# Optimization experiments

Hardware: AMD Instinct MI355X
Metric: run time of the kernel (lower is better)

## Reference

```python
import jax, jax.numpy as jnp
import numpy as np

B, N, CACHE = 2, 2048, 512
D_MODEL, N_HEADS, HEAD_DIM, FF, KSZ = 768, 12, 64, 3072, 31
EPS = 1e-5


def rmsnorm(x, w):
    return x * jax.lax.rsqrt(jnp.mean(x * x, axis=-1, keepdims=True) + EPS) * w


def rope(x, pos):
    # x: [B, T, H, D], pos: [T] (absolute positions incl. cache offset)
    half = x.shape[-1] // 2
    inv = 1.0 / (10000.0 ** (jnp.arange(half, dtype=jnp.float32) / half))
    ang = pos.astype(jnp.float32)[:, None] * inv[None, :]           # [T, half]
    cos = jnp.concatenate([jnp.cos(ang), jnp.cos(ang)], -1)[None, :, None, :]
    sin = jnp.concatenate([jnp.sin(ang), jnp.sin(ang)], -1)[None, :, None, :]
    x1, x2 = x[..., :half], x[..., half:]
    rot = jnp.concatenate([-x2, x1], -1)
    return x * cos + rot * sin


def setup_inputs() -> dict:
    key = jax.random.key(0)
    ks = jax.random.split(key, 16)
    w = lambda k, shape: jax.random.normal(k, shape, jnp.float32) * 0.02
    kk = jax.random.split(ks[15], 16)
    return {
        "x": jax.random.normal(ks[0], (B, N, D_MODEL), jnp.float32),
        "attn_mask": jnp.ones((B, CACHE + N), bool),
        "pad_mask": jnp.zeros((B, N), bool),
        "length": N,
        "cached_kv": jax.random.normal(ks[1], (B, CACHE, 2, N_HEADS, HEAD_DIM), jnp.float32),
        "ff1_norm_w": jnp.ones((D_MODEL,), jnp.float32),
        "ff1_w1": w(ks[2], (D_MODEL, FF)), "ff1_b1": jnp.zeros((FF,), jnp.float32),
        "ff1_w2": w(ks[3], (FF, D_MODEL)), "ff1_b2": jnp.zeros((D_MODEL,), jnp.float32),
        "attn_norm_w": jnp.ones((D_MODEL,), jnp.float32),
        "qkv_w": w(ks[4], (D_MODEL, 3 * N_HEADS * HEAD_DIM)),
        "out_w": w(ks[5], (N_HEADS * HEAD_DIM, D_MODEL)),
        "q_norm_w": jnp.ones((HEAD_DIM,), jnp.float32),
        "k_norm_w": jnp.ones((HEAD_DIM,), jnp.float32),
        "conv_norm_w": jnp.ones((D_MODEL,), jnp.float32),
        "pw1_w": w(ks[6], (D_MODEL, 2 * D_MODEL)), "pw1_b": jnp.zeros((2 * D_MODEL,), jnp.float32),
        "dw_w": w(ks[7], (D_MODEL, KSZ)), "dw_b": jnp.zeros((D_MODEL,), jnp.float32),
        "bn_g": jnp.ones((D_MODEL,), jnp.float32), "bn_b": jnp.zeros((D_MODEL,), jnp.float32),
        "pw2_w": w(ks[8], (D_MODEL, D_MODEL)), "pw2_b": jnp.zeros((D_MODEL,), jnp.float32),
        "ff2_norm_w": jnp.ones((D_MODEL,), jnp.float32),
        "ff2_w1": w(kk[0], (D_MODEL, FF)), "ff2_b1": jnp.zeros((FF,), jnp.float32),
        "ff2_w2": w(kk[1], (FF, D_MODEL)), "ff2_b2": jnp.zeros((D_MODEL,), jnp.float32),
        "out_norm_w": jnp.ones((D_MODEL,), jnp.float32),
    }


def _ff(x, nw, w1, b1, w2, b2):
    h = jax.nn.gelu(rmsnorm(x, nw) @ w1 + b1)        # FusedMLP: gelu(tanh approx)
    return 0.5 * (h @ w2 + b2)                        # Scale(0.5, ...)


def _attention(x, pad_mask, attn_mask, cached_kv, nw, qkv_w, out_w, qnw, knw):
    y = rmsnorm(x, nw)
    y = jnp.where(pad_mask[..., None], 0.0, y)
    qkv = (y @ qkv_w).reshape(B, N, N_HEADS, HEAD_DIM, 3)  # (h d qkv) layout
    q, k, v = qkv[..., 0], qkv[..., 1], qkv[..., 2]
    q = rmsnorm(q, qnw)
    k = rmsnorm(k, knw)
    k_full = jnp.concatenate([cached_kv[:, :, 0], k], axis=1)  # [B, KV, H, D]
    v_full = jnp.concatenate([cached_kv[:, :, 1], v], axis=1)
    kv_to_cache = jnp.stack([k_full, v_full], axis=2)          # [B, KV, 2, H, D]
    kv_len = k_full.shape[1]
    pos = jnp.arange(kv_len)
    k_rot = rope(k_full, pos)
    q_rot = rope(q, pos[kv_len - N:])
    scale = 1.0 / jnp.sqrt(jnp.asarray(HEAD_DIM, jnp.float32))
    scores = jnp.einsum('bqhd,bkhd->bhqk', q_rot, k_rot) * scale
    scores = jnp.where(attn_mask[:, None, None, :], scores, jnp.finfo(scores.dtype).min)
    attn = jax.nn.softmax(scores, axis=-1)
    out = jnp.einsum('bhqk,bkhd->bqhd', attn, v_full).reshape(B, N, N_HEADS * HEAD_DIM)
    out = jnp.where(pad_mask[..., None], 0.0, out)
    return out @ out_w, kv_to_cache


def _conv(x, pad_mask, nw, pw1_w, pw1_b, dw_w, dw_b, bn_g, bn_b, pw2_w, pw2_b):
    y = rmsnorm(x, nw)
    y = jnp.where(pad_mask[..., None], 0.0, y)
    y = y @ pw1_w + pw1_b                             # pointwise conv1
    a, b = jnp.split(y, 2, axis=-1)
    y = a * jax.nn.sigmoid(b)                          # GLU
    rhs = dw_w.T[:, None, :]                           # [K, 1, C] (WIO, depthwise)
    y = jax.lax.conv_general_dilated(
        y, rhs, (1,), [(KSZ // 2, KSZ // 2)],
        dimension_numbers=('NWC', 'WIO', 'NWC'),
        feature_group_count=D_MODEL) + dw_b
    m = jnp.mean(y, axis=(0, 1))                       # batch(re)norm, train-mode stats
    v = jnp.var(y, axis=(0, 1))
    y = (y - m) * jax.lax.rsqrt(v + EPS) * bn_g + bn_b
    y = y * jax.nn.sigmoid(y)                          # SiLU
    return y @ pw2_w + pw2_b


def reference(x, attn_mask, pad_mask, length, cached_kv,
              ff1_norm_w, ff1_w1, ff1_b1, ff1_w2, ff1_b2,
              attn_norm_w, qkv_w, out_w, q_norm_w, k_norm_w,
              conv_norm_w, pw1_w, pw1_b, dw_w, dw_b, bn_g, bn_b, pw2_w, pw2_b,
              ff2_norm_w, ff2_w1, ff2_b1, ff2_w2, ff2_b2, out_norm_w):
    x = _ff(x, ff1_norm_w, ff1_w1, ff1_b1, ff1_w2, ff1_b2) + x
    attn_out, kv_to_cache = _attention(x, pad_mask, attn_mask, cached_kv,
                                       attn_norm_w, qkv_w, out_w, q_norm_w, k_norm_w)
    x = attn_out + x
    # NOTE: source code has no residual add around the conv block
    x = _conv(x, pad_mask, conv_norm_w, pw1_w, pw1_b, dw_w, dw_b, bn_g, bn_b, pw2_w, pw2_b)
    x = _ff(x, ff2_norm_w, ff2_w1, ff2_b1, ff2_w2, ff2_b2) + x
    x = rmsnorm(x, out_norm_w)
    return x, kv_to_cache
```

## Files before the change

### kernel.cpp

```cpp
#include <hip/hip_runtime.h>
#include <hip/hip_bf16.h>
#include <math.h>

namespace {
constexpr int Bc   = 2;
constexpr int Nn   = 2048;
constexpr int CACHE= 512;
constexpr int KVL  = 2560;
constexpr int DM   = 768;
constexpr int NH   = 12;
constexpr int HD   = 64;
constexpr int FFD  = 3072;
constexpr int RR   = Bc * Nn;
}
#define EPSF 1e-5f

typedef unsigned short u16;
typedef __bf16 bf16x8 __attribute__((ext_vector_type(8)));
typedef float  f32x4  __attribute__((ext_vector_type(4)));
typedef u16    u16x8  __attribute__((ext_vector_type(8)));
typedef u16    u16x4  __attribute__((ext_vector_type(4)));

#define GPTR(p) ((const __attribute__((address_space(1))) void*)(p))
#define LPTR(p) ((__attribute__((address_space(3))) void*)(p))

__device__ __forceinline__ float geluf(float x) {
  float x3 = x * x * x;
  float t  = tanhf(0.7978845608028654f * (x + 0.044715f * x3));
  return 0.5f * x * (1.0f + t);
}
__device__ __forceinline__ float sigmoidf_(float x) {
  return 1.0f / (1.0f + __expf(-x));
}
__device__ __forceinline__ u16 f2bf(float x) {
  union { float f; unsigned u; } v; v.f = x;
  unsigned r = (v.u + 0x7fffu + ((v.u >> 16) & 1u)) >> 16;
  return (u16)r;
}
__device__ __forceinline__ float bf2f(u16 u) {
  union { unsigned u; float f; } v; v.u = ((unsigned)u) << 16;
  return v.f;
}

template<bool BF>
__global__ __launch_bounds__(256) void k_rmsnorm2(const float* __restrict__ in,
                                                  const float* __restrict__ w,
                                                  void* __restrict__ outv, int D) {
  const int row = blockIdx.x;
  const float* x = in + (size_t)row * D;
  float ss = 0.f;
  for (int i = threadIdx.x; i < D; i += 256) { float v = x[i]; ss = fmaf(v, v, ss); }
  __shared__ float red[5];
#pragma unroll
  for (int off = 32; off > 0; off >>= 1) ss += __shfl_down(ss, off, 64);
  if ((threadIdx.x & 63) == 0) red[threadIdx.x >> 6] = ss;
  __syncthreads();
  if (threadIdx.x == 0) red[4] = red[0] + red[1] + red[2] + red[3];
  __syncthreads();
  const float scale = rsqrtf(red[4] * (1.0f / (float)D) + EPSF);
  for (int i = threadIdx.x; i < D; i += 256) {
    const float v = x[i] * scale * w[i];
    if (BF) ((u16*)outv)[(size_t)row * D + i] = f2bf(v);
    else    ((float*)outv)[(size_t)row * D + i] = v;
  }
}

__global__ __launch_bounds__(256) void k_wt(const float* __restrict__ W,
                                            u16* __restrict__ Wt, int K, int N) {
  __shared__ __align__(16) u16 T[64][72];
  const int nb = blockIdx.x * 64;
  const int kb = blockIdx.y * 64;
#pragma unroll
  for (int p = 0; p < 4; ++p) {
    const int r = p * 16 + (threadIdx.x >> 4);
    const int c = (threadIdx.x & 15) * 4;
    float4 v = *(const float4*)(W + (size_t)(kb + r) * N + nb + c);
    T[c + 0][r] = f2bf(v.x); T[c + 1][r] = f2bf(v.y);
    T[c + 2][r] = f2bf(v.z); T[c + 3][r] = f2bf(v.w);
  }
  __syncthreads();
  const int cc = (threadIdx.x & 7) * 8;
#pragma unroll
  for (int p = 0; p < 2; ++p) {
    const int rr = p * 32 + (threadIdx.x >> 3);
    *(u16x8*)(Wt + (size_t)(nb + rr) * K + kb + cc) = *(const u16x8*)&T[rr][cc];
  }
}

template<int BN, int MODE, bool OUTBF>
__global__ __launch_bounds__(256) void k_gemm_mfma(const u16* __restrict__ A,
                                                   const u16* __restrict__ Wt,
                                                   const float* __restrict__ bias,
                                                   const float* __restrict__ res,
                                                   void* __restrict__ Cv,
                                                   int K, int Nc) {
  constexpr int BM = 128, BK = 64;
  constexpr int CT = BN / 32;
  __shared__ __align__(16) u16 As[BM * BK];
  __shared__ __align__(16) u16 Bs[BN * BK];
  const int lane = threadIdx.x & 63;
  const int w    = threadIdx.x >> 6;
  const int rowBase = blockIdx.y * BM;
  const int colBase = blockIdx.x * BN;
  const int l15 = lane & 15, quad = lane >> 4;
  const int wr = w >> 1, wc = w & 1;
  const int sw = l15 & 7;

  f32x4 acc[4][CT];
#pragma unroll
  for (int i = 0; i < 4; ++i)
#pragma unroll
    for (int j = 0; j < CT; ++j) acc[i][j] = (f32x4){0.f, 0.f, 0.f, 0.f};

  for (int k0 = 0; k0 < K; k0 += BK) {
#pragma unroll
    for (int s = 0; s < 4; ++s) {
      const int cbase = (w * 4 + s) * 64;
      const int c = cbase + lane;
      const int r = c >> 3;
      const int kc = (c & 7) ^ (r & 7);
      __builtin_amdgcn_global_load_lds(
          GPTR(A + (size_t)(rowBase + r) * K + k0 + kc * 8),
          LPTR((char*)As + (size_t)cbase * 16), 16, 0, 0);
    }
#pragma unroll
    for (int s = 0; s < BN / 32; ++s) {
      const int cbase = (w * (BN / 32) + s) * 64;
      const int c = cbase + lane;
      const int r = c >> 3;
      const int kc = (c & 7) ^ (r & 7);
      __builtin_amdgcn_global_load_lds(
          GPTR(Wt + (size_t)(colBase + r) * K + k0 + kc * 8),
          LPTR((char*)Bs + (size_t)cbase * 16), 16, 0, 0);
    }
    __syncthreads();

#pragma unroll
    for (int kk = 0; kk < 2; ++kk) {
      bf16x8 aF[4], bF[CT];
#pragma unroll
      for (int rt = 0; rt < 4; ++rt) {
        const int row = wr * 64 + rt * 16 + l15;
        aF[rt] = *(const bf16x8*)&As[row * BK + (((kk * 4 + quad) ^ sw) * 8)];
      }
#pragma unroll
      for (int ct = 0; ct < CT; ++ct) {
        const int row = wc * (BN / 2) + ct * 16 + l15;
        bF[ct] = *(const bf16x8*)&Bs[row * BK + (((kk * 4 + quad) ^ sw) * 8)];
      }
#pragma unroll
      for (int rt = 0; rt < 4; ++rt)
#pragma unroll
        for (int ct = 0; ct < CT; ++ct)
          acc[rt][ct] = __builtin_amdgcn_mfma_f32_16x16x32_bf16(aF[rt], bF[ct],
                                                                acc[rt][ct], 0, 0, 0);
    }
    __syncthreads();
  }

#pragma unroll
  for (int ct = 0; ct < CT; ++ct) {
    const int col = colBase + wc * (BN / 2) + ct * 16 + l15;
    const float bv = bias ? bias[col] : 0.f;
#pragma unroll
    for (int rt = 0; rt < 4; ++rt) {
#pragma unroll
      for (int r = 0; r < 4; ++r) {
        const int row = rowBase + wr * 64 + rt * 16 + quad * 4 + r;
        float v = acc[rt][ct][r] + bv;
        if (MODE == 1) v = geluf(v);
        else if (MODE == 2) v = 0.5f * v + res[(size_t)row * Nc + col];
        else if (MODE == 3) v = v + res[(size_t)row * Nc + col];
        if (OUTBF) ((u16*)Cv)[(size_t)row * Nc + col] = f2bf(v);
        else       ((float*)Cv)[(size_t)row * Nc + col] = v;
      }
    }
  }
}

__global__ __launch_bounds__(768) void k_qkv_post(const float* __restrict__ qkv,
                                                  const float* __restrict__ qw,
                                                  const float* __restrict__ kw,
                                                  u16* __restrict__ qbf,
                                                  u16* __restrict__ krotbf,
                                                  float* __restrict__ kvout) {
  const int row = blockIdx.x;
  const int b = row >> 11;
  const int n = row & 2047;
  const int h = threadIdx.x >> 6;
  const int d = threadIdx.x & 63;
  const float* src = qkv + (size_t)row * (3 * DM) + h * 192 + d * 3;
  const float q = src[0], k = src[1], v = src[2];
  float sq = q * q, sk = k * k;
#pragma unroll
  for (int off = 32; off > 0; off >>= 1) {
    sq += __shfl_xor(sq, off, 64);
    sk += __shfl_xor(sk, off, 64);
  }
  const float qs = rsqrtf(sq * (1.0f / 64.0f) + EPSF);
  const float ks = rsqrtf(sk * (1.0f / 64.0f) + EPSF);
  const float qn = q * qs * qw[d];
  const float kn = k * ks * kw[d];
  const size_t kvbase = ((size_t)b * KVL + (CACHE + n)) * (2 * DM) + h * 64 + d;
  kvout[kvbase] = kn;
  kvout[kvbase + DM] = v;
  const int j = d & 31;
  const float inv = powf(10000.0f, -(float)j * (1.0f / 32.0f));
  float s, c;
  sincosf((float)(CACHE + n) * inv, &s, &c);
  const float oq = __shfl_xor(qn, 32, 64);
  const float ok = __shfl_xor(kn, 32, 64);
  const float rq = (d < 32) ? -oq : oq;
  const float rk = (d < 32) ? -ok : ok;
  qbf[((size_t)row * NH + h) * 64 + d] = f2bf((qn * c + rq * s) * 0.125f);
  krotbf[((size_t)(b * KVL + CACHE + n) * NH + h) * 64 + d] = f2bf(kn * c + rk * s);
}

__global__ __launch_bounds__(768) void k_cache_prep(const float* __restrict__ cached,
                                                    float* __restrict__ kvout,
                                                    u16* __restrict__ krotbf) {
  const int row = blockIdx.x;
  const int b = row / CACHE, t = row - b * CACHE;
  const int h = threadIdx.x >> 6;
  const int d = threadIdx.x & 63;
  const float k = cached[((size_t)row * 2 + 0) * DM + h * 64 + d];
  const float v = cached[((size_t)row * 2 + 1) * DM + h * 64 + d];
  const size_t kb = ((size_t)b * KVL + t) * (2 * DM) + h * 64 + d;
  kvout[kb] = k;
  kvout[kb + DM] = v;
  const int j = d & 31;
  const float inv = powf(10000.0f, -(float)j * (1.0f / 32.0f));
  float s, c;
  sincosf((float)t * inv, &s, &c);
  const float ok = __shfl_xor(k, 32, 64);
  const float rk = (d < 32) ? -ok : ok;
  krotbf[((size_t)(b * KVL + t) * NH + h) * 64 + d] = f2bf(k * c + rk * s);
}

__global__ __launch_bounds__(256) void k_vt(const float* __restrict__ kvout,
                                            u16* __restrict__ vtbf) {
  __shared__ __align__(16) u16 T[64][72];
  const int bh = blockIdx.x / 40;
  const int tb = blockIdx.x % 40;
  const int b = bh / NH, h = bh % NH;
  const int t0 = tb * 64;
  {
    const int tloc = threadIdx.x >> 2;
    const int dg = (threadIdx.x & 3) * 16;
    const float* src = kvout + ((size_t)b * KVL + t0 + tloc) * (2 * DM) + DM + h * 64 + dg;
    float4 v0 = *(const float4*)(src);
    float4 v1 = *(const float4*)(src + 4);
    float4 v2 = *(const float4*)(src + 8);
    float4 v3 = *(const float4*)(src + 12);
    T[dg + 0][tloc] = f2bf(v0.x);  T[dg + 1][tloc] = f2bf(v0.y);
    T[dg + 2][tloc] = f2bf(v0.z);  T[dg + 3][tloc] = f2bf(v0.w);
    T[dg + 4][tloc] = f2bf(v1.x);  T[dg + 5][tloc] = f2bf(v1.y);
    T[dg + 6][tloc] = f2bf(v1.z);  T[dg + 7][tloc] = f2bf(v1.w);
    T[dg + 8][tloc] = f2bf(v2.x);  T[dg + 9][tloc] = f2bf(v2.y);
    T[dg + 10][tloc] = f2bf(v2.z); T[dg + 11][tloc] = f2bf(v2.w);
    T[dg + 12][tloc] = f2bf(v3.x); T[dg + 13][tloc] = f2bf(v3.y);
    T[dg + 14][tloc] = f2bf(v3.z); T[dg + 15][tloc] = f2bf(v3.w);
  }
  __syncthreads();
  const int d = threadIdx.x >> 2;
  const int kg = (threadIdx.x & 3) * 16;
  u16x8 a = *(const u16x8*)&T[d][kg];
  u16x8 b8 = *(const u16x8*)&T[d][kg + 8];
  u16* dst = vtbf + ((size_t)(b * NH + h) * 64 + d) * KVL + t0 + kg;
  *(u16x8*)dst = a;
  *(u16x8*)(dst + 8) = b8;
}

__global__ __launch_bounds__(256) void k_attn2(const u16* __restrict__ qbf,
                                               const u16* __restrict__ krotbf,
                                               const u16* __restrict__ vtbf,
                                               float* __restrict__ Apart,
                                               float* __restrict__ lpart) {
  __shared__ __align__(16) u16 Ks[64 * 64];
  __shared__ __align__(16) u16 Vs[64 * 64];
  __shared__ __align__(16) u16 Ps[4][16][80];
  const int lane = threadIdx.x & 63;
  const int wid  = threadIdx.x >> 6;
  const int sp   = blockIdx.x & 1;
  const int rest = blockIdx.x >> 1;
  const int qblk = rest & 31;
  const int bh   = rest >> 5;
  const int b = bh / NH, h = bh % NH;
  const int q0 = qblk * 64 + wid * 16;
  const int l15 = lane & 15;
  const int quad = lane >> 4;
  const int sw = l15 & 7;

  const u16* qp = qbf + ((size_t)(b * Nn + q0 + l15) * NH + h) * 64 + quad * 8;
  const bf16x8 bQ0 = *(const bf16x8*)qp;
  const bf16x8 bQ1 = *(const bf16x8*)(qp + 32);

  f32x4 O[4] = {};
  float l_lane = 0.f;

  const u16* kbase = krotbf + ((size_t)b * KVL * NH + h) * 64;
  const u16* vbase = vtbf + ((size_t)(b * NH + h) * 64) * KVL;

  const int tbeg = sp * (KVL / 2);
  for (int t0 = tbeg; t0 < tbeg + KVL / 2; t0 += 64) {
    __syncthreads();
#pragma unroll
    for (int it = 0; it < 2; ++it) {
      const int cbase = (wid * 2 + it) * 64;
      const int c = cbase + lane;
      const int r = c >> 3;
      const int kc = (c & 7) ^ (r & 7);
      __builtin_amdgcn_global_load_lds(
          GPTR(kbase + (size_t)(t0 + r) * (NH * 64) + kc * 8),
          LPTR((char*)Ks + (size_t)cbase * 16), 16, 0, 0);
      __builtin_amdgcn_global_load_lds(
          GPTR(vbase + (size_t)r * KVL + t0 + kc * 8),
          LPTR((char*)Vs + (size_t)cbase * 16), 16, 0, 0);
    }
    __syncthreads();

#pragma unroll
    for (int nt = 0; nt < 4; ++nt) {
      const int krow = nt * 16 + l15;
      const bf16x8 aK0 = *(const bf16x8*)&Ks[krow * 64 + ((quad ^ sw) * 8)];
      const bf16x8 aK1 = *(const bf16x8*)&Ks[krow * 64 + (((4 + quad) ^ sw) * 8)];
      f32x4 cc = {};
      cc = __builtin_amdgcn_mfma_f32_16x16x32_bf16(aK0, bQ0, cc, 0, 0, 0);
      cc = __builtin_amdgcn_mfma_f32_16x16x32_bf16(aK1, bQ1, cc, 0, 0, 0);
      const float p0 = __expf(cc[0]);
      const float p1 = __expf(cc[1]);
      const float p2 = __expf(cc[2]);
      const float p3 = __expf(cc[3]);
      l_lane += (p0 + p1) + (p2 + p3);
      uint2 pk;
      pk.x = (unsigned)f2bf(p0) | ((unsigned)f2bf(p1) << 16);
      pk.y = (unsigned)f2bf(p2) | ((unsigned)f2bf(p3) << 16);
      *(uint2*)&Ps[wid][l15][nt * 16 + quad * 4] = pk;
    }
    asm volatile("s_waitcnt lgkmcnt(0)" ::: "memory");

#pragma unroll
    for (int kt = 0; kt < 2; ++kt) {
      const bf16x8 bP = *(const bf16x8*)&Ps[wid][l15][kt * 32 + quad * 8];
#pragma unroll
      for (int ot = 0; ot < 4; ++ot) {
        const int vrow = ot * 16 + l15;
        const bf16x8 aV = *(const bf16x8*)&Vs[vrow * 64 + (((kt * 4 + quad) ^ sw) * 8)];
        O[ot] = __builtin_amdgcn_mfma_f32_16x16x32_bf16(aV, bP, O[ot], 0, 0, 0);
      }
    }
  }

  l_lane += __shfl_xor(l_lane, 16, 64);
  l_lane += __shfl_xor(l_lane, 32, 64);
  const int sbh = (sp * Bc + b) * NH + h;
  if (quad == 0) lpart[(size_t)sbh * Nn + q0 + l15] = l_lane;
  float* ap = Apart + ((size_t)sbh * 64) * Nn + q0 + l15;
#pragma unroll
  for (int ot = 0; ot < 4; ++ot)
#pragma unroll
    for (int r = 0; r < 4; ++r)
      ap[(size_t)(ot * 16 + quad * 4 + r) * Nn] = O[ot][r];
}

__global__ __launch_bounds__(256) void k_attn_merge(const float* __restrict__ Apart,
                                                    const float* __restrict__ lpart,
                                                    u16* __restrict__ attnout) {
  __shared__ float T[64][65];
  __shared__ float il[64];
  const int qt = blockIdx.x & 31;
  const int bh = blockIdx.x >> 5;
  const int b = bh / NH, h = bh % NH;
  const int q0 = qt * 64;
  const int bh0 = b * NH + h;
  const int bh1 = (Bc + b) * NH + h;
  if (threadIdx.x < 64) {
    const int q = threadIdx.x;
    il[q] = 1.0f / (lpart[(size_t)bh0 * Nn + q0 + q] + lpart[(size_t)bh1 * Nn + q0 + q]);
  }
  const float* a0 = Apart + ((size_t)bh0 * 64) * Nn + q0;
  const float* a1 = Apart + ((size_t)bh1 * 64) * Nn + q0;
#pragma unroll
  for (int p = 0; p < 16; ++p) {
    const int idx = p * 256 + threadIdx.x;
    const int d = idx >> 6, q = idx & 63;
    T[q][d] = a0[(size_t)d * Nn + q] + a1[(size_t)d * Nn + q];
  }
  __syncthreads();
#pragma unroll
  for (int p = 0; p < 16; ++p) {
    const int idx = p * 256 + threadIdx.x;
    const int q = idx >> 6, d = idx & 63;
    attnout[((size_t)(b * Nn + q0 + q)) * DM + h * 64 + d] = f2bf(T[q][d] * il[q]);
  }
}

__global__ __launch_bounds__(256) void k_dwconv2(const u16* __restrict__ pw1,
                                                 const float* __restrict__ w,
                                                 const float* __restrict__ bsd,
                                                 float* __restrict__ out,
                                                 float* __restrict__ stats) {
  __shared__ float S[94][68];
  __shared__ float Wl[31][64];
  const int cb = blockIdx.x * 64;
  const int n0 = blockIdx.y * 64;
  const int b  = blockIdx.z;
  for (int idx = threadIdx.x; idx < 94 * 16; idx += 256) {
    const int r = idx >> 4, cg = (idx & 15) * 4;
    const int n = n0 - 15 + r;
    float4 v = make_float4(0.f, 0.f, 0.f, 0.f);
    if (n >= 0 && n < Nn) {
      const u16* p = pw1 + ((size_t)(b * Nn + n)) * (2 * DM) + cb + cg;
      u16x4 av = *(const u16x4*)(p);
      u16x4 gv = *(const u16x4*)(p + DM);
      v.x = bf2f(av[0]) * sigmoidf_(bf2f(gv[0]));
      v.y = bf2f(av[1]) * sigmoidf_(bf2f(gv[1]));
      v.z = bf2f(av[2]) * sigmoidf_(bf2f(gv[2]));
      v.w = bf2f(av[3]) * sigmoidf_(bf2f(gv[3]));
    }
    *(float4*)&S[r][cg] = v;
  }
  for (int idx = threadIdx.x; idx < 31 * 64; idx += 256) {
    const int c = idx & 63, tap = idx >> 6;
    Wl[tap][c] = w[(size_t)(cb + c) * 31 + tap];
  }
  __syncthreads();

  const int cg  = (threadIdx.x & 15) * 4;
  const int nl0 = threadIdx.x >> 4;
  const float4 b4 = *(const float4*)(bsd + cb + cg);
  float sum[4] = {0.f, 0.f, 0.f, 0.f};
  float sq[4]  = {0.f, 0.f, 0.f, 0.f};
#pragma unroll
  for (int p = 0; p < 4; ++p) {
    const int nl = p * 16 + nl0;
    float a0 = b4.x, a1 = b4.y, a2 = b4.z, a3 = b4.w;
#pragma unroll
    for (int t = 0; t < 31; ++t) {
      const float4 sv = *(const float4*)&S[nl + t][cg];
      const float4 wv = *(const float4*)&Wl[t][cg & 63];
      a0 = fmaf(sv.x, wv.x, a0); a1 = fmaf(sv.y, wv.y, a1);
      a2 = fmaf(sv.z, wv.z, a2); a3 = fmaf(sv.w, wv.w, a3);
    }
    *(float4*)(out + ((size_t)(b * Nn + n0 + nl)) * DM + cb + cg) =
        make_float4(a0, a1, a2, a3);
    sum[0] += a0; sum[1] += a1; sum[2] += a2; sum[3] += a3;
    sq[0] = fmaf(a0, a0, sq[0]); sq[1] = fmaf(a1, a1, sq[1]);
    sq[2] = fmaf(a2, a2, sq[2]); sq[3] = fmaf(a3, a3, sq[3]);
  }
  __syncthreads();
  *(float4*)&S[nl0][cg]      = make_float4(sum[0], sum[1], sum[2], sum[3]);
  *(float4*)&S[16 + nl0][cg] = make_float4(sq[0], sq[1], sq[2], sq[3]);
  __syncthreads();
  if (threadIdx.x < 64) {
    const int c = threadIdx.x;
    float s = 0.f, q = 0.f;
#pragma unroll
    for (int i = 0; i < 16; ++i) { s += S[i][c]; q += S[16 + i][c]; }
    atomicAdd(&stats[cb + c], s);
    atomicAdd(&stats[DM + cb + c], q);
  }
}

__global__ __launch_bounds__(256) void k_zero(float* __restrict__ p, int n) {
  const int i = blockIdx.x * 256 + threadIdx.x;
  if (i < n) p[i] = 0.f;
}

__global__ __launch_bounds__(256) void k_bn_apply(const float* __restrict__ x,
                                                  const float* __restrict__ stats,
                                                  const float* __restrict__ g,
                                                  const float* __restrict__ bb,
                                                  u16* __restrict__ out) {
  const int idx = blockIdx.x * 256 + threadIdx.x;
  const int c = idx % DM;
  const float mean = stats[c] * (1.0f / (float)RR);
  const float var = stats[DM + c] * (1.0f / (float)RR) - mean * mean;
  float y = (x[idx] - mean) * rsqrtf(var + EPSF) * g[c] + bb[c];
  out[idx] = f2bf(y * sigmoidf_(y));
}

extern "C" void kernel_launch(void* const* d_in, const int* in_sizes, int n_in,
                              void* d_out, int out_size, void* d_ws, size_t ws_size,
                              hipStream_t stream) {
  const float* x       = (const float*)d_in[0];
  const float* cached  = (const float*)d_in[4];
  const float* ff1_nw  = (const float*)d_in[5];
  const float* ff1_w1  = (const float*)d_in[6];
  const float* ff1_b1  = (const float*)d_in[7];
  const float* ff1_w2  = (const float*)d_in[8];
  const float* ff1_b2  = (const float*)d_in[9];
  const float* attn_nw = (const float*)d_in[10];
  const float* qkv_w   = (const float*)d_in[11];
  const float* out_w   = (const float*)d_in[12];
  const float* q_nw    = (const float*)d_in[13];
  const float* k_nw    = (const float*)d_in[14];
  const float* conv_nw = (const float*)d_in[15];
  const float* pw1_w   = (const float*)d_in[16];
  const float* pw1_b   = (const float*)d_in[17];
  const float* dw_w    = (const float*)d_in[18];
  const float* dw_b    = (const float*)d_in[19];
  const float* bn_g    = (const float*)d_in[20];
  const float* bn_b    = (const float*)d_in[21];
  const float* pw2_w   = (const float*)d_in[22];
  const float* pw2_b   = (const float*)d_in[23];
  const float* ff2_nw  = (const float*)d_in[24];
  const float* ff2_w1  = (const float*)d_in[25];
  const float* ff2_b1  = (const float*)d_in[26];
  const float* ff2_w2  = (const float*)d_in[27];
  const float* ff2_b2  = (const float*)d_in[28];
  const float* out_nw  = (const float*)d_in[29];

  float* out_x  = (float*)d_out;
  float* out_kv = out_x + (size_t)RR * DM;

  u16* wt_ff1w1 = (u16*)d_ws;
  u16* wt_ff1w2 = wt_ff1w1 + (size_t)3072 * 768;
  u16* wt_qkv   = wt_ff1w2 + (size_t)768 * 3072;
  u16* wt_out   = wt_qkv   + (size_t)2304 * 768;
  u16* wt_pw1   = wt_out   + (size_t)768 * 768;
  u16* wt_pw2   = wt_pw1   + (size_t)1536 * 768;
  u16* wt_ff2w1 = wt_pw2   + (size_t)768 * 768;
  u16* wt_ff2w2 = wt_ff2w1 + (size_t)3072 * 768;
  u16* abuf     = wt_ff2w2 + (size_t)768 * 3072;
  u16* hbuf     = abuf + (size_t)RR * DM;
  float* xA     = (float*)(hbuf + (size_t)RR * FFD);
  float* xB     = xA + (size_t)RR * DM;
  float* qkvbuf = xB + (size_t)RR * DM;
  u16* qbf      = (u16*)(qkvbuf + (size_t)RR * 3 * DM);
  u16* krotbf   = qbf + (size_t)RR * DM;
  u16* vtbf     = krotbf + (size_t)Bc * KVL * DM;
  float* bn_stats = (float*)(vtbf + (size_t)Bc * KVL * DM);
  float* Apart  = (float*)hbuf;
  u16* attnout  = (u16*)qkvbuf;
  float* lpart  = qkvbuf + (size_t)RR * DM;
  float* dwout  = qkvbuf;
  u16* bnout    = (u16*)(qkvbuf + (size_t)RR * DM);

  const dim3 blk(256);
  k_wt<<<dim3(48, 12), blk, 0, stream>>>(ff1_w1, wt_ff1w1, DM, FFD);
  k_wt<<<dim3(12, 48), blk, 0, stream>>>(ff1_w2, wt_ff1w2, FFD, DM);
  k_wt<<<dim3(36, 12), blk, 0, stream>>>(qkv_w, wt_qkv, DM, 3 * DM);
  k_wt<<<dim3(12, 12), blk, 0, stream>>>(out_w, wt_out, DM, DM);
  k_wt<<<dim3(24, 12), blk, 0, stream>>>(pw1_w, wt_pw1, DM, 2 * DM);
  k_wt<<<dim3(12, 12), blk, 0, stream>>>(pw2_w, wt_pw2, DM, DM);
  k_wt<<<dim3(48, 12), blk, 0, stream>>>(ff2_w1, wt_ff2w1, DM, FFD);
  k_wt<<<dim3(12, 48), blk, 0, stream>>>(ff2_w2, wt_ff2w2, FFD, DM);

  k_rmsnorm2<true><<<RR, blk, 0, stream>>>(x, ff1_nw, abuf, DM);
  k_gemm_mfma<128, 1, true><<<dim3(FFD / 128, RR / 128), blk, 0, stream>>>(
      abuf, wt_ff1w1, ff1_b1, nullptr, hbuf, DM, FFD);
  k_gemm_mfma<64, 2, false><<<dim3(DM / 64, RR / 128), blk, 0, stream>>>(
      hbuf, wt_ff1w2, ff1_b2, x, xA, FFD, DM);
  k_rmsnorm2<true><<<RR, blk, 0, stream>>>(xA, attn_nw, abuf, DM);
  k_gemm_mfma<128, 0, false><<<dim3(3 * DM / 128, RR / 128), blk, 0, stream>>>(
      abuf, wt_qkv, nullptr, nullptr, qkvbuf, DM, 3 * DM);
  k_qkv_post<<<RR, 768, 0, stream>>>(qkvbuf, q_nw, k_nw, qbf, krotbf, out_kv);
  k_cache_prep<<<Bc * CACHE, 768, 0, stream>>>(cached, out_kv, krotbf);
  k_vt<<<Bc * NH * (KVL / 64), blk, 0, stream>>>(out_kv, vtbf);
  k_attn2<<<Bc * NH * (Nn / 64) * 2, blk, 0, stream>>>(qbf, krotbf, vtbf, Apart, lpart);
  k_attn_merge<<<Bc * NH * (Nn / 64), blk, 0, stream>>>(Apart, lpart, attnout);
  k_gemm_mfma<64, 3, false><<<dim3(DM / 64, RR / 128), blk, 0, stream>>>(
      attnout, wt_out, nullptr, xA, xB, DM, DM);
  k_rmsnorm2<true><<<RR, blk, 0, stream>>>(xB, conv_nw, abuf, DM);
  k_gemm_mfma<128, 0, true><<<dim3(2 * DM / 128, RR / 128), blk, 0, stream>>>(
      abuf, wt_pw1, pw1_b, nullptr, hbuf, DM, 2 * DM);
  k_zero<<<6, blk, 0, stream>>>(bn_stats, 2 * DM);
  k_dwconv2<<<dim3(DM / 64, Nn / 64, Bc), blk, 0, stream>>>(hbuf, dw_w, dw_b,
                                                            dwout, bn_stats);
  k_bn_apply<<<RR * DM / 256, blk, 0, stream>>>(dwout, bn_stats, bn_g, bn_b, bnout);
  k_gemm_mfma<64, 0, false><<<dim3(DM / 64, RR / 128), blk, 0, stream>>>(
      bnout, wt_pw2, pw2_b, nullptr, xA, DM, DM);
  k_rmsnorm2<true><<<RR, blk, 0, stream>>>(xA, ff2_nw, abuf, DM);
  k_gemm_mfma<128, 1, true><<<dim3(FFD / 128, RR / 128), blk, 0, stream>>>(
      abuf, wt_ff2w1, ff2_b1, nullptr, hbuf, DM, FFD);
  k_gemm_mfma<64, 2, false><<<dim3(DM / 64, RR / 128), blk, 0, stream>>>(
      hbuf, wt_ff2w2, ff2_b2, xA, xB, FFD, DM);
  k_rmsnorm2<false><<<RR, blk, 0, stream>>>(xB, out_nw, out_x, DM);
}
```

Measured before the change: 602.9 us.

## Double-buffer attention K/V tiles and use hardware exp/rcp/sin intrinsics

The attention kernel now double-buffers K and V tiles in LDS: it prefetches the next tile with global_load_lds while computing on the current one, and uses vmcnt waits and raw barriers instead of two __syncthreads per iteration. The P staging buffer drops its padding in favour of an XOR swizzle, bf16 packing uses v_cvt_pk_bf16_f32, and the PV MFMA section runs at raised wave priority. Softmax switches to exp2 with log2(e) folded into the Q scale. GELU, sigmoid and RoPE sin/cos are replaced by raw v_exp/v_rcp/v_sin/v_cos approximations, which trades some accuracy for fewer instructions.

```diff
diff --git a/kernel.cpp b/kernel.cpp
--- a/kernel.cpp
+++ b/kernel.cpp
@@ -24,13 +24,25 @@
 #define GPTR(p) ((const __attribute__((address_space(1))) void*)(p))
 #define LPTR(p) ((__attribute__((address_space(3))) void*)(p))
 
+__device__ __forceinline__ float fast_exp2(float a) {
+  float e;
+  asm("v_exp_f32 %0, %1" : "=v"(e) : "v"(a));
+  return e;
+}
+__device__ __forceinline__ float fast_rcp(float x) {
+  float r;
+  asm("v_rcp_f32 %0, %1" : "=v"(r) : "v"(x));
+  return r;
+}
 __device__ __forceinline__ float geluf(float x) {
-  float x3 = x * x * x;
-  float t  = tanhf(0.7978845608028654f * (x + 0.044715f * x3));
+  const float u = 0.7978845608028654f * x * (1.0f + 0.044715f * x * x);
+  const float e = fast_exp2(u * 2.885390081777927f);
+  const float t = (e - 1.0f) * fast_rcp(e + 1.0f);
   return 0.5f * x * (1.0f + t);
 }
 __device__ __forceinline__ float sigmoidf_(float x) {
-  return 1.0f / (1.0f + __expf(-x));
+  const float e = fast_exp2(-x * 1.4426950408889634f);
+  return fast_rcp(1.0f + e);
 }
 __device__ __forceinline__ u16 f2bf(float x) {
   union { float f; unsigned u; } v; v.f = x;
@@ -40,6 +52,13 @@
 __device__ __forceinline__ float bf2f(u16 u) {
   union { unsigned u; float f; } v; v.u = ((unsigned)u) << 16;
   return v.f;
+}
+__device__ __forceinline__ void rope_sc(float pos, int j, float* s, float* c) {
+  const float e = fast_exp2(-(float)j * 0.41524101186092028f);
+  const float rev = pos * (e * 0.15915494309189535f);
+  const float fr = rev - floorf(rev);
+  asm("v_sin_f32 %0, %1" : "=v"(*s) : "v"(fr));
+  asm("v_cos_f32 %0, %1" : "=v"(*c) : "v"(fr));
 }
 
 template<bool BF>
@@ -205,14 +224,13 @@
   kvout[kvbase] = kn;
   kvout[kvbase + DM] = v;
   const int j = d & 31;
-  const float inv = powf(10000.0f, -(float)j * (1.0f / 32.0f));
   float s, c;
-  sincosf((float)(CACHE + n) * inv, &s, &c);
+  rope_sc((float)(CACHE + n), j, &s, &c);
   const float oq = __shfl_xor(qn, 32, 64);
   const float ok = __shfl_xor(kn, 32, 64);
   const float rq = (d < 32) ? -oq : oq;
   const float rk = (d < 32) ? -ok : ok;
-  qbf[((size_t)row * NH + h) * 64 + d] = f2bf((qn * c + rq * s) * 0.125f);
+  qbf[((size_t)row * NH + h) * 64 + d] = f2bf((qn * c + rq * s) * 0.18033688011112042f);
   krotbf[((size_t)(b * KVL + CACHE + n) * NH + h) * 64 + d] = f2bf(kn * c + rk * s);
 }
 
@@ -229,9 +247,8 @@
   kvout[kb] = k;
   kvout[kb + DM] = v;
   const int j = d & 31;
-  const float inv = powf(10000.0f, -(float)j * (1.0f / 32.0f));
   float s, c;
-  sincosf((float)t * inv, &s, &c);
+  rope_sc((float)t, j, &s, &c);
   const float ok = __shfl_xor(k, 32, 64);
   const float rk = (d < 32) ? -ok : ok;
   krotbf[((size_t)(b * KVL + t) * NH + h) * 64 + d] = f2bf(k * c + rk * s);
@@ -276,9 +293,9 @@
                                                const u16* __restrict__ vtbf,
                                                float* __restrict__ Apart,
                                                float* __restrict__ lpart) {
-  __shared__ __align__(16) u16 Ks[64 * 64];
-  __shared__ __align__(16) u16 Vs[64 * 64];
-  __shared__ __align__(16) u16 Ps[4][16][80];
+  __shared__ __align__(16) u16 Ks[2][64 * 64];
+  __shared__ __align__(16) u16 Vs[2][64 * 64];
+  __shared__ __align__(16) u16 Ps[4][16][64];
   const int lane = threadIdx.x & 63;
   const int wid  = threadIdx.x >> 6;
   const int sp   = blockIdx.x & 1;
@@ -294,61 +311,88 @@
   const u16* qp = qbf + ((size_t)(b * Nn + q0 + l15) * NH + h) * 64 + quad * 8;
   const bf16x8 bQ0 = *(const bf16x8*)qp;
   const bf16x8 bQ1 = *(const bf16x8*)(qp + 32);
+  asm volatile("" :: "v"(*(const f32x4*)&bQ0), "v"(*(const f32x4*)&bQ1));
 
   f32x4 O[4] = {};
   float l_lane = 0.f;
 
+  const int c0 = (wid * 2 + 0) * 64 + lane;
+  const int c1 = (wid * 2 + 1) * 64 + lane;
+  const int r0 = c0 >> 3, kc0 = (c0 & 7) ^ (r0 & 7);
+  const int r1 = c1 >> 3, kc1 = (c1 & 7) ^ (r1 & 7);
   const u16* kbase = krotbf + ((size_t)b * KVL * NH + h) * 64;
   const u16* vbase = vtbf + ((size_t)(b * NH + h) * 64) * KVL;
+  const u16* ksrc0 = kbase + (size_t)r0 * (NH * 64) + kc0 * 8;
+  const u16* ksrc1 = kbase + (size_t)r1 * (NH * 64) + kc1 * 8;
+  const u16* vsrc0 = vbase + (size_t)r0 * KVL + kc0 * 8;
+  const u16* vsrc1 = vbase + (size_t)r1 * KVL + kc1 * 8;
+  const size_t kd0 = (size_t)(wid * 2 + 0) * 1024;
+  const size_t kd1 = (size_t)(wid * 2 + 1) * 1024;
+
+  auto stage = [&](int buf, int t0) {
+    char* kd = (char*)Ks[buf];
+    char* vd = (char*)Vs[buf];
+    __builtin_amdgcn_global_load_lds(GPTR(ksrc0 + (size_t)t0 * (NH * 64)),
+                                     LPTR(kd + kd0), 16, 0, 0);
+    __builtin_amdgcn_global_load_lds(GPTR(vsrc0 + t0), LPTR(vd + kd0), 16, 0, 0);
+    __builtin_amdgcn_global_load_lds(GPTR(ksrc1 + (size_t)t0 * (NH * 64)),
+                                     LPTR(kd + kd1), 16, 0, 0);
+    __builtin_amdgcn_global_load_lds(GPTR(vsrc1 + t0), LPTR(vd + kd1), 16, 0, 0);
+  };
 
   const int tbeg = sp * (KVL / 2);
-  for (int t0 = tbeg; t0 < tbeg + KVL / 2; t0 += 64) {
-    __syncthreads();
-#pragma unroll
-    for (int it = 0; it < 2; ++it) {
-      const int cbase = (wid * 2 + it) * 64;
-      const int c = cbase + lane;
-      const int r = c >> 3;
-      const int kc = (c & 7) ^ (r & 7);
-      __builtin_amdgcn_global_load_lds(
-          GPTR(kbase + (size_t)(t0 + r) * (NH * 64) + kc * 8),
-          LPTR((char*)Ks + (size_t)cbase * 16), 16, 0, 0);
-      __builtin_amdgcn_global_load_lds(
-          GPTR(vbase + (size_t)r * KVL + t0 + kc * 8),
-          LPTR((char*)Vs + (size_t)cbase * 16), 16, 0, 0);
-    }
-    __syncthreads();
+  constexpr int NT = (KVL / 2) / 64;
+
+  stage(0, tbeg);
+  for (int i = 0; i < NT; ++i) {
+    const int cur = i & 1;
+    if (i + 1 < NT) {
+      stage(cur ^ 1, tbeg + (i + 1) * 64);
+      asm volatile("s_waitcnt vmcnt(4)" ::: "memory");
+    } else {
+      asm volatile("s_waitcnt vmcnt(0)" ::: "memory");
+    }
+    __builtin_amdgcn_s_barrier();
+    asm volatile("" ::: "memory");
+    const u16* ksc = Ks[cur];
+    const u16* vsc = Vs[cur];
 
 #pragma unroll
     for (int nt = 0; nt < 4; ++nt) {
       const int krow = nt * 16 + l15;
-      const bf16x8 aK0 = *(const bf16x8*)&Ks[krow * 64 + ((quad ^ sw) * 8)];
-      const bf16x8 aK1 = *(const bf16x8*)&Ks[krow * 64 + (((4 + quad) ^ sw) * 8)];
+      const bf16x8 aK0 = *(const bf16x8*)&ksc[krow * 64 + ((quad ^ sw) * 8)];
+      const bf16x8 aK1 = *(const bf16x8*)&ksc[krow * 64 + (((4 + quad) ^ sw) * 8)];
       f32x4 cc = {};
       cc = __builtin_amdgcn_mfma_f32_16x16x32_bf16(aK0, bQ0, cc, 0, 0, 0);
       cc = __builtin_amdgcn_mfma_f32_16x16x32_bf16(aK1, bQ1, cc, 0, 0, 0);
-      const float p0 = __expf(cc[0]);
-      const float p1 = __expf(cc[1]);
-      const float p2 = __expf(cc[2]);
-      const float p3 = __expf(cc[3]);
+      const float p0 = fast_exp2(cc[0]);
+      const float p1 = fast_exp2(cc[1]);
+      const float p2 = fast_exp2(cc[2]);
+      const float p3 = fast_exp2(cc[3]);
       l_lane += (p0 + p1) + (p2 + p3);
-      uint2 pk;
-      pk.x = (unsigned)f2bf(p0) | ((unsigned)f2bf(p1) << 16);
-      pk.y = (unsigned)f2bf(p2) | ((unsigned)f2bf(p3) << 16);
-      *(uint2*)&Ps[wid][l15][nt * 16 + quad * 4] = pk;
+      unsigned w0, w1;
+      asm("v_cvt_pk_bf16_f32 %0, %1, %2" : "=v"(w0) : "v"(p0), "v"(p1));
+      asm("v_cvt_pk_bf16_f32 %0, %1, %2" : "=v"(w1) : "v"(p2), "v"(p3));
+      uint2 pk; pk.x = w0; pk.y = w1;
+      const int pg = (nt * 2 + (quad >> 1)) ^ sw;
+      *(uint2*)&Ps[wid][l15][pg * 8 + (quad & 1) * 4] = pk;
     }
     asm volatile("s_waitcnt lgkmcnt(0)" ::: "memory");
 
+    __builtin_amdgcn_s_setprio(1);
 #pragma unroll
     for (int kt = 0; kt < 2; ++kt) {
-      const bf16x8 bP = *(const bf16x8*)&Ps[wid][l15][kt * 32 + quad * 8];
+      const bf16x8 bP = *(const bf16x8*)&Ps[wid][l15][((kt * 4 + quad) ^ sw) * 8];
 #pragma unroll
       for (int ot = 0; ot < 4; ++ot) {
         const int vrow = ot * 16 + l15;
-        const bf16x8 aV = *(const bf16x8*)&Vs[vrow * 64 + (((kt * 4 + quad) ^ sw) * 8)];
+        const bf16x8 aV = *(const bf16x8*)&vsc[vrow * 64 + (((kt * 4 + quad) ^ sw) * 8)];
         O[ot] = __builtin_amdgcn_mfma_f32_16x16x32_bf16(aV, bP, O[ot], 0, 0, 0);
       }
     }
+    __builtin_amdgcn_s_setprio(0);
+    asm volatile("" ::: "memory");
+    __builtin_amdgcn_s_barrier();
   }
 
   l_lane += __shfl_xor(l_lane, 16, 64);
```

Measured after the change: 575.6 us. 1.05x faster.
